# Performance work log

Hardware: AMD Instinct MI355X
Metric: run time of the kernel (lower is better)

The kernel has to match this reference:

```python
import jax, jax.numpy as jnp
import numpy as np

TOKEN_DIM = 768
HIDDEN_DIM = 384
PATCH_SCALE = 2
SELECTED_RATIO = 0.15


def setup_inputs() -> dict:
    key = jax.random.key(0)
    ks = jax.random.split(key, 12)
    B, T, D = 32, 1024, TOKEN_DIM
    Thr = T * PATCH_SCALE * PATCH_SCALE  # 4096
    flat_dim = D * PATCH_SCALE * PATCH_SCALE  # 3072
    H = HIDDEN_DIM
    s = lambda fan_in: 1.0 / np.sqrt(fan_in)
    inp = {
        "base_tokens": jax.random.normal(ks[0], (B, T, D), jnp.float32),
        "highres_tokens": jax.random.normal(ks[1], (B, Thr, D), jnp.float32),
        "selection_scores": jax.random.normal(ks[2], (B, T), jnp.float32),
        # local_refine: Linear(flat_dim,H) -> GELU -> Linear(H,D)
        "W1": jax.random.uniform(ks[3], (flat_dim, H), jnp.float32, -s(flat_dim), s(flat_dim)),
        "b1": jax.random.uniform(ks[4], (H,), jnp.float32, -s(flat_dim), s(flat_dim)),
        "W2": jax.random.uniform(ks[5], (H, D), jnp.float32, -s(H), s(H)),
        "b2": jax.random.uniform(ks[6], (D,), jnp.float32, -s(H), s(H)),
        # blend_gate: Linear(2D+1,H) -> SiLU -> Linear(H,1)
        "Wg1": jax.random.uniform(ks[7], (2 * D + 1, H), jnp.float32, -s(2 * D + 1), s(2 * D + 1)),
        "bg1": jax.random.uniform(ks[8], (H,), jnp.float32, -s(2 * D + 1), s(2 * D + 1)),
        "Wg2": jax.random.uniform(ks[9], (H, 1), jnp.float32, -s(H), s(H)),
        "bg2": jax.random.uniform(ks[10], (1,), jnp.float32, -s(H), s(H)),
    }
    return inp


def reference(base_tokens, highres_tokens, selection_scores,
              W1, b1, W2, b2, Wg1, bg1, Wg2, bg2):
    B, T, D = base_tokens.shape
    S = PATCH_SCALE
    g = int(round(np.sqrt(T)))  # coarse grid side
    # strided patch reshape: [B, g, S, g, S, D] -> [B, g, g, S, S, D] -> [B, T, S*S*D]
    local = highres_tokens.reshape(B, g, S, g, S, D)
    local = local.transpose(0, 1, 3, 2, 4, 5).reshape(B, T, S * S * D)
    # local refine MLP (exact-erf GELU matches torch nn.GELU default)
    h = jax.nn.gelu(jnp.einsum('btf,fh->bth', local, W1) + b1, approximate=False)
    refined_local = jnp.einsum('bth,hd->btd', h, W2) + b2
    # blend gate
    gate_in = jnp.concatenate([base_tokens, refined_local, selection_scores[..., None]], axis=-1)
    hg = jax.nn.silu(jnp.einsum('btf,fh->bth', gate_in, Wg1) + bg1)
    gate = jax.nn.sigmoid(jnp.einsum('bth,ho->bto', hg, Wg2) + bg2)  # [B, T, 1]
    # top-k selection mask (static k)
    topk = max(1, int(round(T * SELECTED_RATIO)))
    topk_idx = jax.lax.top_k(selection_scores, topk)[1]  # [B, k]
    mask = jnp.zeros((B, T), base_tokens.dtype).at[jnp.arange(B)[:, None], topk_idx].set(1.0)
    refined = base_tokens + mask[..., None] * gate * (refined_local - base_tokens)
    return refined
```

## Files before the change

### kernel.cpp

```cpp
#include <hip/hip_runtime.h>
#include <cstdint>

#define NB    32
#define NTOK  1024
#define D_    768
#define NHR   4096
#define HID   384
#define KSEL  154
#define MSEL  4928
#define MT_   77
#define FLAT  3072

typedef short  s16x8 __attribute__((ext_vector_type(8)));
typedef unsigned short u16x8 __attribute__((ext_vector_type(8)));
typedef unsigned short u16x4 __attribute__((ext_vector_type(4)));
typedef float  f32x4 __attribute__((ext_vector_type(4)));

__device__ inline unsigned short f2bf(float f) {
    uint32_t u = __builtin_bit_cast(uint32_t, f);
    u += 0x7FFFu + ((u >> 16) & 1u);
    return (unsigned short)(u >> 16);
}
__device__ inline float bf2f(unsigned short h) {
    uint32_t u = ((uint32_t)h) << 16;
    return __builtin_bit_cast(float, u);
}
__device__ inline s16x8 cvt8(const float* __restrict__ p) {
    float4 v0 = *(const float4*)p, v1 = *(const float4*)(p + 4);
    s16x8 r;
    r[0]=(short)f2bf(v0.x); r[1]=(short)f2bf(v0.y); r[2]=(short)f2bf(v0.z); r[3]=(short)f2bf(v0.w);
    r[4]=(short)f2bf(v1.x); r[5]=(short)f2bf(v1.y); r[6]=(short)f2bf(v1.z); r[7]=(short)f2bf(v1.w);
    return r;
}

#define OFF_SEL   0
#define OFF_RMAP  32768
#define OFF_GPART 163840
#define OFF_W1T   401408
#define OFF_W2T   2760704
#define OFF_WG1T  3350528
#define OFF_ABASE 4530176
#define OFF_H     12099584
#define OFF_RL    15884288
#define DOUT_P0   32505856
#define PSTRIDE   (MSEL * HID)

__global__ __launch_bounds__(1024) void prep_kernel(
    const float* __restrict__ scores, int* __restrict__ sel, int* __restrict__ rmap,
    const float* __restrict__ W1, const float* __restrict__ W2, const float* __restrict__ Wg1,
    unsigned short* __restrict__ W1t, unsigned short* __restrict__ W2t,
    unsigned short* __restrict__ Wg1t)
{
    __shared__ float s[NTOK];
    __shared__ int cnt;
    __shared__ unsigned short T[4][64][66];
    const int bid = blockIdx.x;
    if (bid < NB) {
        const int b = bid;
        const int t = threadIdx.x;
        s[t] = scores[b * NTOK + t];
        if (t == 0) cnt = 0;
        __syncthreads();
        float v = s[t];
        int rank = 0;
        for (int j = 0; j < NTOK; ++j) {
            float vj = s[j];
            rank += (vj > v) || (vj == v && j < t);
        }
        int rm = -1;
        if (rank < KSEL) {
            int pos = atomicAdd(&cnt, 1);
            rm = b * KSEL + pos;
            sel[rm] = t;
        }
        rmap[b * NTOK + t] = rm;
    } else {
        const int g = threadIdx.x >> 8;
        const int tid = threadIdx.x & 255;
        const int tile = (bid - NB) * 4 + g;
        const float* src; unsigned short* dst; int K, N, kt, nt;
        if (tile < 288)      { src = W1;  dst = W1t;  K = FLAT; N = HID; nt = tile % 6;  kt = tile / 6;  }
        else if (tile < 360) { int l = tile - 288; src = W2;  dst = W2t;  K = HID;  N = D_;  nt = l % 12; kt = l / 12; }
        else                 { int l = tile - 360; src = Wg1; dst = Wg1t; K = 1536; N = HID; nt = l % 6;  kt = l / 6;  }
        const int k0 = kt * 64, n0 = nt * 64;
        {
            const int ln = tid & 63, kc = tid >> 6;
            #pragma unroll
            for (int j = 0; j < 16; ++j)
                T[g][ln][kc * 16 + j] = f2bf(src[(uint64_t)(k0 + kc * 16 + j) * N + n0 + ln]);
        }
        __syncthreads();
        {
            const int row = tid >> 2, c0 = (tid & 3) * 16;
            u16x8 v0, v1;
            #pragma unroll
            for (int p = 0; p < 8; ++p) { v0[p] = T[g][row][c0 + p]; v1[p] = T[g][row][c0 + 8 + p]; }
            *(u16x8*)(dst + (uint64_t)(n0 + row) * K + k0 + c0) = v0;
            *(u16x8*)(dst + (uint64_t)(n0 + row) * K + k0 + c0 + 8) = v1;
        }
    }
}

__global__ __launch_bounds__(256) void gather_kernel(
    const int* __restrict__ sel, const float* __restrict__ highres,
    const float* __restrict__ base,
    unsigned short* __restrict__ Aloc, unsigned short* __restrict__ Abase) {
    const int r = blockIdx.x;
    const int b = r / KSEL;
    const int t = sel[r];
    const int gy = t >> 5, gx = t & 31;
    for (int ch = threadIdx.x; ch < 480; ch += 256) {
        if (ch < 384) {
            int k8 = ch * 8;
            int p = k8 / D_;
            int col = k8 - p * D_;
            int hr = (gy * 2 + (p >> 1)) * 64 + gx * 2 + (p & 1);
            s16x8 v = cvt8(highres + ((uint64_t)b * NHR + hr) * D_ + col);
            *(s16x8*)(Aloc + (uint64_t)r * FLAT + k8) = v;
        } else {
            int col = (ch - 384) * 8;
            s16x8 v = cvt8(base + ((uint64_t)b * NTOK + t) * D_ + col);
            *(s16x8*)(Abase + (uint64_t)r * D_ + col) = v;
        }
    }
}

template <int MODE>
__global__ __launch_bounds__(256) void gemm_mfma(
    const unsigned short* __restrict__ A0,
    const unsigned short* __restrict__ A1,
    const unsigned short* __restrict__ Bt,
    const float* __restrict__ bias,
    const int* __restrict__ sel,
    const float* __restrict__ scores,
    const float* __restrict__ WgLast,
    const float* __restrict__ Wg2,
    void* __restrict__ Cout,
    float* __restrict__ Pout,
    float* __restrict__ gpart)
{
    constexpr int K = MODE == 0 ? FLAT : (MODE == 1 ? HID : 2 * D_);
    constexpr int N = MODE == 1 ? D_ : HID;
    constexpr int BN = (MODE == 2) ? 64 : 128;
    constexpr int NFRAG = BN / 32;
    constexpr int NT = N / BN;
    constexpr int KLEN = (MODE == 0) ? 1024 : K;
    constexpr int NSTEP = KLEN / 64;
    constexpr int NSPLIT = (MODE == 0) ? 3 : 1;

    const int lin = blockIdx.x;
    const int xcd = lin & 7;
    int j = lin >> 3;
    const int ntile = j % NT; j /= NT;
    const int mhi = j % 10;
    const int split = j / 10;
    const int mt = mhi * 8 + xcd;
    if (mt >= MT_) return;
    const int m0 = mt * 64;
    const int n0 = ntile * BN;
    const int kb = split * KLEN;

    __shared__ unsigned short As[2][64 * 64];
    __shared__ unsigned short Bs[2][BN * 64];
    __shared__ float scv[64];

    const int tid = threadIdx.x;
    const int lane = tid & 63;
    const int wid = tid >> 6;
    const int wm = wid >> 1;
    const int wn = wid & 1;

    if (MODE == 2 && tid < 64) {
        int r = m0 + tid, b = r / KSEL, t = sel[r];
        scv[tid] = scores[b * NTOK + t];
    }

    const int sr0 = tid >> 3;
    const int sc0 = tid & 7;

    s16x8 aR[2], bR[NFRAG];
    auto loadTile = [&](int k0) {
        #pragma unroll
        for (int half = 0; half < 2; ++half) {
            int r = sr0 + half * 32;
            int k = k0 + sc0 * 8;
            const unsigned short* p;
            if (MODE == 0)      p = A0 + (uint64_t)(m0 + r) * FLAT + k;
            else if (MODE == 1) p = A0 + (uint64_t)(m0 + r) * HID + k;
            else {
                p = (k < D_) ? (A0 + (uint64_t)(m0 + r) * D_ + k)
                             : (A1 + (uint64_t)(m0 + r) * D_ + (k - D_));
            }
            aR[half] = *(const s16x8*)p;
        }
        #pragma unroll
        for (int it = 0; it < NFRAG; ++it) {
            int r = it * 32 + sr0;
            bR[it] = *(const s16x8*)(Bt + (uint64_t)(n0 + r) * K + k0 + sc0 * 8);
        }
    };
    auto writeTile = [&](int buf) {
        #pragma unroll
        for (int half = 0; half < 2; ++half) {
            int r = sr0 + half * 32;
            int c = sc0 ^ (r & 7);
            *(s16x8*)&As[buf][r * 64 + c * 8] = aR[half];
        }
        #pragma unroll
        for (int it = 0; it < NFRAG; ++it) {
            int r = it * 32 + sr0;
            int c = sc0 ^ (r & 7);
            *(s16x8*)&Bs[buf][r * 64 + c * 8] = bR[it];
        }
    };

    f32x4 acc[2][NFRAG];
    #pragma unroll
    for (int i = 0; i < 2; ++i)
        #pragma unroll
        for (int jj = 0; jj < NFRAG; ++jj) acc[i][jj] = (f32x4){0.f, 0.f, 0.f, 0.f};

    loadTile(kb);
    writeTile(0);
    __syncthreads();
    if (NSTEP > 1) loadTile(kb + 64);

    int cur = 0;
    for (int t = 0; t < NSTEP; ++t) {
        #pragma unroll
        for (int kk = 0; kk < 2; ++kk) {
            s16x8 af[2], bfr[NFRAG];
            #pragma unroll
            for (int i = 0; i < 2; ++i) {
                int row = wm * 32 + i * 16 + (lane & 15);
                int cch = (kk * 4 + (lane >> 4)) ^ (row & 7);
                af[i] = *(const s16x8*)&As[cur][row * 64 + cch * 8];
            }
            #pragma unroll
            for (int jj = 0; jj < NFRAG; ++jj) {
                int nrow = wn * (BN / 2) + jj * 16 + (lane & 15);
                int cch = (kk * 4 + (lane >> 4)) ^ (nrow & 7);
                bfr[jj] = *(const s16x8*)&Bs[cur][nrow * 64 + cch * 8];
            }
            #pragma unroll
            for (int i = 0; i < 2; ++i)
                #pragma unroll
                for (int jj = 0; jj < NFRAG; ++jj)
                    acc[i][jj] = __builtin_amdgcn_mfma_f32_16x16x32_bf16(af[i], bfr[jj], acc[i][jj], 0, 0, 0);
        }
        if (t + 1 < NSTEP) {
            writeTile(cur ^ 1);
            __syncthreads();
            if (t + 2 < NSTEP) loadTile(kb + (t + 2) * 64);
            cur ^= 1;
        }
    }

    if (MODE == 2) {
        float wg2v[2] = { Wg2[n0 + wn * 32 + (lane & 15)],
                          Wg2[n0 + wn * 32 + 16 + (lane & 15)] };
        float psum[2][4];
        #pragma unroll
        for (int i = 0; i < 2; ++i)
            #pragma unroll
            for (int reg = 0; reg < 4; ++reg) psum[i][reg] = 0.f;
        #pragma unroll
        for (int i = 0; i < 2; ++i) {
            #pragma unroll
            for (int jj = 0; jj < 2; ++jj) {
                #pragma unroll
                for (int reg = 0; reg < 4; ++reg) {
                    int m = m0 + wm * 32 + i * 16 + (lane >> 4) * 4 + reg;
                    int n = n0 + wn * 32 + jj * 16 + (lane & 15);
                    float x = acc[i][jj][reg] + bias[n] + scv[m - m0] * WgLast[n];
                    x = x / (1.0f + __expf(-x));
                    psum[i][reg] += x * wg2v[jj];
                }
            }
        }
        #pragma unroll
        for (int mask = 1; mask < 16; mask <<= 1)
            #pragma unroll
            for (int i = 0; i < 2; ++i)
                #pragma unroll
                for (int reg = 0; reg < 4; ++reg)
                    psum[i][reg] += __shfl_xor(psum[i][reg], mask);
        if ((lane & 15) == 0) {
            #pragma unroll
            for (int i = 0; i < 2; ++i)
                #pragma unroll
                for (int reg = 0; reg < 4; ++reg) {
                    int m = m0 + wm * 32 + i * 16 + (lane >> 4) * 4 + reg;
                    gpart[m * 12 + ntile * 2 + wn] = psum[i][reg];
                }
        }
        return;
    }
    float* P = (MODE == 0) ? (Pout + (uint64_t)split * PSTRIDE) : nullptr;
    #pragma unroll
    for (int i = 0; i < 2; ++i)
        #pragma unroll
        for (int jj = 0; jj < NFRAG; ++jj)
            #pragma unroll
            for (int reg = 0; reg < 4; ++reg) {
                int m = m0 + wm * 32 + i * 16 + (lane >> 4) * 4 + reg;
                int n = n0 + wn * (BN / 2) + jj * 16 + (lane & 15);
                if (MODE == 0) {
                    P[(uint64_t)m * HID + n] = acc[i][jj][reg];
                } else {
                    float x = acc[i][jj][reg] + bias[n];
                    ((unsigned short*)Cout)[(uint64_t)m * D_ + n] = f2bf(x);
                }
            }
}

__global__ __launch_bounds__(256) void combine_kernel(
    const float* __restrict__ P, const float* __restrict__ b1,
    unsigned short* __restrict__ h)
{
    const int idx = (blockIdx.x * 256 + threadIdx.x) * 8;
    const int col = idx % HID;
    float4 a0 = *(const float4*)(P + idx),               a1 = *(const float4*)(P + idx + 4);
    float4 c0 = *(const float4*)(P + PSTRIDE + idx),     c1 = *(const float4*)(P + PSTRIDE + idx + 4);
    float4 d0 = *(const float4*)(P + 2 * PSTRIDE + idx), d1 = *(const float4*)(P + 2 * PSTRIDE + idx + 4);
    float4 bb0 = *(const float4*)(b1 + col), bb1 = *(const float4*)(b1 + col + 4);
    float xs[8] = { a0.x + c0.x + d0.x + bb0.x, a0.y + c0.y + d0.y + bb0.y,
                    a0.z + c0.z + d0.z + bb0.z, a0.w + c0.w + d0.w + bb0.w,
                    a1.x + c1.x + d1.x + bb1.x, a1.y + c1.y + d1.y + bb1.y,
                    a1.z + c1.z + d1.z + bb1.z, a1.w + c1.w + d1.w + bb1.w };
    u16x8 v;
    #pragma unroll
    for (int p = 0; p < 8; ++p) {
        float x = xs[p];
        x = 0.5f * x * (1.0f + erff(x * 0.70710678118654752f));
        v[p] = f2bf(x);
    }
    *(u16x8*)(h + idx) = v;
}

__global__ __launch_bounds__(256) void finalize_kernel(
    const int* __restrict__ rmap,
    const float* __restrict__ gpart, const float* __restrict__ bg2,
    const float* __restrict__ base, const unsigned short* __restrict__ rl,
    float* __restrict__ out)
{
    const int lane = threadIdx.x & 63;
    const int row = blockIdx.x * 4 + (threadIdx.x >> 6);
    const int rm = rmap[row];

    const uint64_t bo = (uint64_t)row * D_;
    const float4* b4 = (const float4*)(base + bo);
    float4* o4 = (float4*)(out + bo);

    if (rm < 0) {
        #pragma unroll
        for (int i = 0; i < 3; ++i) o4[lane + 64 * i] = b4[lane + 64 * i];
        return;
    }
    const float4* gp = (const float4*)(gpart + (uint64_t)rm * 12);
    float4 g0 = gp[0], g1 = gp[1], g2 = gp[2];
    float sum = g0.x + g0.y + g0.z + g0.w + g1.x + g1.y + g1.z + g1.w
              + g2.x + g2.y + g2.z + g2.w + bg2[0];
    float gate = 1.0f / (1.0f + __expf(-sum));

    const u16x4* r4 = (const u16x4*)(rl + (uint64_t)rm * D_);
    #pragma unroll
    for (int i = 0; i < 3; ++i) {
        int idx = lane + 64 * i;
        float4 bb = b4[idx];
        u16x4 rr = r4[idx];
        float4 oo;
        oo.x = bb.x + gate * (bf2f(rr[0]) - bb.x);
        oo.y = bb.y + gate * (bf2f(rr[1]) - bb.y);
        oo.z = bb.z + gate * (bf2f(rr[2]) - bb.z);
        oo.w = bb.w + gate * (bf2f(rr[3]) - bb.w);
        o4[idx] = oo;
    }
}

extern "C" void kernel_launch(void* const* d_in, const int* in_sizes, int n_in,
                              void* d_out, int out_size, void* d_ws, size_t ws_size,
                              hipStream_t stream) {
    const float* base   = (const float*)d_in[0];
    const float* hires  = (const float*)d_in[1];
    const float* scores = (const float*)d_in[2];
    const float* W1  = (const float*)d_in[3];
    const float* b1  = (const float*)d_in[4];
    const float* W2  = (const float*)d_in[5];
    const float* b2  = (const float*)d_in[6];
    const float* Wg1 = (const float*)d_in[7];
    const float* bg1 = (const float*)d_in[8];
    const float* Wg2 = (const float*)d_in[9];
    const float* bg2 = (const float*)d_in[10];
    float* out = (float*)d_out;

    char* ws = (char*)d_ws;
    int*            sel   = (int*)(ws + OFF_SEL);
    int*            rmap  = (int*)(ws + OFF_RMAP);
    float*          gpart = (float*)(ws + OFF_GPART);
    unsigned short* W1t   = (unsigned short*)(ws + OFF_W1T);
    unsigned short* W2t   = (unsigned short*)(ws + OFF_W2T);
    unsigned short* Wg1t  = (unsigned short*)(ws + OFF_WG1T);
    unsigned short* Abase = (unsigned short*)(ws + OFF_ABASE);
    unsigned short* h     = (unsigned short*)(ws + OFF_H);
    unsigned short* rl    = (unsigned short*)(ws + OFF_RL);
    unsigned short* Aloc  = (unsigned short*)d_out;
    float*          P0    = (float*)((char*)d_out + DOUT_P0);

    prep_kernel<<<dim3(NB + 126), dim3(1024), 0, stream>>>(scores, sel, rmap,
                                                           W1, W2, Wg1, W1t, W2t, Wg1t);
    gather_kernel<<<dim3(MSEL), dim3(256), 0, stream>>>(sel, hires, base, Aloc, Abase);
    gemm_mfma<0><<<dim3(8 * 10 * 3 * 3), dim3(256), 0, stream>>>(
        Aloc, nullptr, W1t, nullptr, nullptr, nullptr, nullptr, nullptr, nullptr, P0, nullptr);
    combine_kernel<<<dim3(924), dim3(256), 0, stream>>>(P0, b1, h);
    gemm_mfma<1><<<dim3(8 * 10 * 6), dim3(256), 0, stream>>>(
        h, nullptr, W2t, b2, nullptr, nullptr, nullptr, nullptr, rl, nullptr, nullptr);
    gemm_mfma<2><<<dim3(8 * 10 * 6), dim3(256), 0, stream>>>(
        Abase, rl, Wg1t, bg1, sel, scores, Wg1 + (uint64_t)1536 * HID, Wg2,
        nullptr, nullptr, gpart);
    finalize_kernel<<<dim3(NB * NTOK / 4), dim3(256), 0, stream>>>(rmap, gpart, bg2, base, rl, out);
}
```

Baseline: 148.4 us.

## Fuse selected-token gather and bf16 conversion into GEMM A-tile loads

Result: slower. 152.3 us (+2.6%).

```diff
diff --git a/kernel.cpp b/kernel.cpp
--- a/kernel.cpp
+++ b/kernel.cpp
@@ -39,10 +39,8 @@
 #define OFF_W1T   401408
 #define OFF_W2T   2760704
 #define OFF_WG1T  3350528
-#define OFF_ABASE 4530176
-#define OFF_H     12099584
-#define OFF_RL    15884288
-#define DOUT_P0   32505856
+#define OFF_H     4530176
+#define OFF_RL    8314880
 #define PSTRIDE   (MSEL * HID)
 
 __global__ __launch_bounds__(1024) void prep_kernel(
@@ -101,34 +99,10 @@
     }
 }
 
-__global__ __launch_bounds__(256) void gather_kernel(
-    const int* __restrict__ sel, const float* __restrict__ highres,
-    const float* __restrict__ base,
-    unsigned short* __restrict__ Aloc, unsigned short* __restrict__ Abase) {
-    const int r = blockIdx.x;
-    const int b = r / KSEL;
-    const int t = sel[r];
-    const int gy = t >> 5, gx = t & 31;
-    for (int ch = threadIdx.x; ch < 480; ch += 256) {
-        if (ch < 384) {
-            int k8 = ch * 8;
-            int p = k8 / D_;
-            int col = k8 - p * D_;
-            int hr = (gy * 2 + (p >> 1)) * 64 + gx * 2 + (p & 1);
-            s16x8 v = cvt8(highres + ((uint64_t)b * NHR + hr) * D_ + col);
-            *(s16x8*)(Aloc + (uint64_t)r * FLAT + k8) = v;
-        } else {
-            int col = (ch - 384) * 8;
-            s16x8 v = cvt8(base + ((uint64_t)b * NTOK + t) * D_ + col);
-            *(s16x8*)(Abase + (uint64_t)r * D_ + col) = v;
-        }
-    }
-}
-
 template <int MODE>
 __global__ __launch_bounds__(256) void gemm_mfma(
-    const unsigned short* __restrict__ A0,
-    const unsigned short* __restrict__ A1,
+    const float* __restrict__ Araw,
+    const unsigned short* __restrict__ Abf,
     const unsigned short* __restrict__ Bt,
     const float* __restrict__ bias,
     const int* __restrict__ sel,
@@ -146,7 +120,6 @@
     constexpr int NT = N / BN;
     constexpr int KLEN = (MODE == 0) ? 1024 : K;
     constexpr int NSTEP = KLEN / 64;
-    constexpr int NSPLIT = (MODE == 0) ? 3 : 1;
 
     const int lin = blockIdx.x;
     const int xcd = lin & 7;
@@ -162,6 +135,7 @@
 
     __shared__ unsigned short As[2][64 * 64];
     __shared__ unsigned short Bs[2][BN * 64];
+    __shared__ uint32_t offT[64 * 4];
     __shared__ float scv[64];
 
     const int tid = threadIdx.x;
@@ -170,10 +144,23 @@
     const int wm = wid >> 1;
     const int wn = wid & 1;
 
-    if (MODE == 2 && tid < 64) {
-        int r = m0 + tid, b = r / KSEL, t = sel[r];
-        scv[tid] = scores[b * NTOK + t];
-    }
+    if (tid < 64) {
+        int r = m0 + tid;
+        if (MODE == 0) {
+            int b = r / KSEL, t = sel[r];
+            int gy = t >> 5, gx = t & 31;
+            #pragma unroll
+            for (int p = 0; p < 4; ++p) {
+                int hr = (gy * 2 + (p >> 1)) * 64 + gx * 2 + (p & 1);
+                offT[tid * 4 + p] = (uint32_t)(b * NHR + hr) * D_;
+            }
+        } else if (MODE == 2) {
+            int b = r / KSEL, t = sel[r];
+            offT[tid * 4] = (uint32_t)(b * NTOK + t) * D_;
+            scv[tid] = scores[b * NTOK + t];
+        }
+    }
+    if (MODE != 1) __syncthreads();
 
     const int sr0 = tid >> 3;
     const int sc0 = tid & 7;
@@ -184,14 +171,15 @@
         for (int half = 0; half < 2; ++half) {
             int r = sr0 + half * 32;
             int k = k0 + sc0 * 8;
-            const unsigned short* p;
-            if (MODE == 0)      p = A0 + (uint64_t)(m0 + r) * FLAT + k;
-            else if (MODE == 1) p = A0 + (uint64_t)(m0 + r) * HID + k;
-            else {
-                p = (k < D_) ? (A0 + (uint64_t)(m0 + r) * D_ + k)
-                             : (A1 + (uint64_t)(m0 + r) * D_ + (k - D_));
-            }
-            aR[half] = *(const s16x8*)p;
+            if (MODE == 0) {
+                int p = k0 / D_;
+                aR[half] = cvt8(Araw + offT[r * 4 + p] + (k - p * D_));
+            } else if (MODE == 1) {
+                aR[half] = *(const s16x8*)(Abf + (uint64_t)(m0 + r) * HID + k);
+            } else {
+                if (k < D_) aR[half] = cvt8(Araw + offT[r * 4] + k);
+                else        aR[half] = *(const s16x8*)(Abf + (uint64_t)(m0 + r) * D_ + (k - D_));
+            }
         }
         #pragma unroll
         for (int it = 0; it < NFRAG; ++it) {
@@ -401,22 +389,19 @@
     unsigned short* W1t   = (unsigned short*)(ws + OFF_W1T);
     unsigned short* W2t   = (unsigned short*)(ws + OFF_W2T);
     unsigned short* Wg1t  = (unsigned short*)(ws + OFF_WG1T);
-    unsigned short* Abase = (unsigned short*)(ws + OFF_ABASE);
     unsigned short* h     = (unsigned short*)(ws + OFF_H);
     unsigned short* rl    = (unsigned short*)(ws + OFF_RL);
-    unsigned short* Aloc  = (unsigned short*)d_out;
-    float*          P0    = (float*)((char*)d_out + DOUT_P0);
+    float*          P0    = (float*)d_out;
 
     prep_kernel<<<dim3(NB + 126), dim3(1024), 0, stream>>>(scores, sel, rmap,
                                                            W1, W2, Wg1, W1t, W2t, Wg1t);
-    gather_kernel<<<dim3(MSEL), dim3(256), 0, stream>>>(sel, hires, base, Aloc, Abase);
     gemm_mfma<0><<<dim3(8 * 10 * 3 * 3), dim3(256), 0, stream>>>(
-        Aloc, nullptr, W1t, nullptr, nullptr, nullptr, nullptr, nullptr, nullptr, P0, nullptr);
+        hires, nullptr, W1t, nullptr, sel, nullptr, nullptr, nullptr, nullptr, P0, nullptr);
     combine_kernel<<<dim3(924), dim3(256), 0, stream>>>(P0, b1, h);
     gemm_mfma<1><<<dim3(8 * 10 * 6), dim3(256), 0, stream>>>(
-        h, nullptr, W2t, b2, nullptr, nullptr, nullptr, nullptr, rl, nullptr, nullptr);
+        nullptr, h, W2t, b2, nullptr, nullptr, nullptr, nullptr, rl, nullptr, nullptr);
     gemm_mfma<2><<<dim3(8 * 10 * 6), dim3(256), 0, stream>>>(
-        Abase, rl, Wg1t, bg1, sel, scores, Wg1 + (uint64_t)1536 * HID, Wg2,
+        base, rl, Wg1t, bg1, sel, scores, Wg1 + (uint64_t)1536 * HID, Wg2,
         nullptr, nullptr, gpart);
     finalize_kernel<<<dim3(NB * NTOK / 4), dim3(256), 0, stream>>>(rmap, gpart, bg2, base, rl, out);
 }
```

## Overlap base-to-output copy with GEMM kernels via extra copy blocks

Applied to the files above, without the earlier changes.

After: 157.6 us. 1.06x slower.

```diff
diff --git a/kernel.cpp b/kernel.cpp
--- a/kernel.cpp
+++ b/kernel.cpp
@@ -42,7 +42,7 @@
 #define OFF_ABASE 4530176
 #define OFF_H     12099584
 #define OFF_RL    15884288
-#define DOUT_P0   32505856
+#define PBASE     77955072
 #define PSTRIDE   (MSEL * HID)
 
 __global__ __launch_bounds__(1024) void prep_kernel(
@@ -137,7 +137,9 @@
     const float* __restrict__ Wg2,
     void* __restrict__ Cout,
     float* __restrict__ Pout,
-    float* __restrict__ gpart)
+    float* __restrict__ gpart,
+    const float* __restrict__ CpySrc,
+    float* __restrict__ CpyDst)
 {
     constexpr int K = MODE == 0 ? FLAT : (MODE == 1 ? HID : 2 * D_);
     constexpr int N = MODE == 1 ? D_ : HID;
@@ -146,9 +148,22 @@
     constexpr int NT = N / BN;
     constexpr int KLEN = (MODE == 0) ? 1024 : K;
     constexpr int NSTEP = KLEN / 64;
-    constexpr int NSPLIT = (MODE == 0) ? 3 : 1;
+    constexpr int GB  = (MODE == 0) ? 720 : 480;
+    constexpr int CB  = (MODE == 0) ? 768 : 512;
+    constexpr int CLO = (MODE == 0) ? 9856 : (MODE == 1 ? 0 : 25376);
+    constexpr int CNR = (MODE == 0) ? 15520 : (MODE == 1 ? 9856 : 7392);
 
     const int lin = blockIdx.x;
+    if (lin >= GB) {
+        const int cb = lin - GB;
+        const float4* src = (const float4*)CpySrc + (uint64_t)CLO * 192;
+        float4* dst = (float4*)CpyDst + (uint64_t)CLO * 192;
+        const int n4 = CNR * 192;
+        for (int idx = cb * 256 + threadIdx.x; idx < n4; idx += CB * 256)
+            dst[idx] = src[idx];
+        return;
+    }
+
     const int xcd = lin & 7;
     int j = lin >> 3;
     const int ntile = j % NT; j /= NT;
@@ -338,32 +353,27 @@
     *(u16x8*)(h + idx) = v;
 }
 
-__global__ __launch_bounds__(256) void finalize_kernel(
-    const int* __restrict__ rmap,
+__global__ __launch_bounds__(256) void blend_kernel(
+    const int* __restrict__ sel,
     const float* __restrict__ gpart, const float* __restrict__ bg2,
     const float* __restrict__ base, const unsigned short* __restrict__ rl,
     float* __restrict__ out)
 {
     const int lane = threadIdx.x & 63;
-    const int row = blockIdx.x * 4 + (threadIdx.x >> 6);
-    const int rm = rmap[row];
-
-    const uint64_t bo = (uint64_t)row * D_;
-    const float4* b4 = (const float4*)(base + bo);
-    float4* o4 = (float4*)(out + bo);
-
-    if (rm < 0) {
-        #pragma unroll
-        for (int i = 0; i < 3; ++i) o4[lane + 64 * i] = b4[lane + 64 * i];
-        return;
-    }
-    const float4* gp = (const float4*)(gpart + (uint64_t)rm * 12);
+    const int r = blockIdx.x * 4 + (threadIdx.x >> 6);
+    const int b = r / KSEL;
+    const int t = sel[r];
+
+    const float4* gp = (const float4*)(gpart + (uint64_t)r * 12);
     float4 g0 = gp[0], g1 = gp[1], g2 = gp[2];
     float sum = g0.x + g0.y + g0.z + g0.w + g1.x + g1.y + g1.z + g1.w
               + g2.x + g2.y + g2.z + g2.w + bg2[0];
     float gate = 1.0f / (1.0f + __expf(-sum));
 
-    const u16x4* r4 = (const u16x4*)(rl + (uint64_t)rm * D_);
+    const uint64_t bo = ((uint64_t)b * NTOK + t) * D_;
+    const float4* b4 = (const float4*)(base + bo);
+    const u16x4* r4 = (const u16x4*)(rl + (uint64_t)r * D_);
+    float4* o4 = (float4*)(out + bo);
     #pragma unroll
     for (int i = 0; i < 3; ++i) {
         int idx = lane + 64 * i;
@@ -405,18 +415,20 @@
     unsigned short* h     = (unsigned short*)(ws + OFF_H);
     unsigned short* rl    = (unsigned short*)(ws + OFF_RL);
     unsigned short* Aloc  = (unsigned short*)d_out;
-    float*          P0    = (float*)((char*)d_out + DOUT_P0);
+    float*          P0    = (float*)((char*)d_out + PBASE);
 
     prep_kernel<<<dim3(NB + 126), dim3(1024), 0, stream>>>(scores, sel, rmap,
                                                            W1, W2, Wg1, W1t, W2t, Wg1t);
     gather_kernel<<<dim3(MSEL), dim3(256), 0, stream>>>(sel, hires, base, Aloc, Abase);
-    gemm_mfma<0><<<dim3(8 * 10 * 3 * 3), dim3(256), 0, stream>>>(
-        Aloc, nullptr, W1t, nullptr, nullptr, nullptr, nullptr, nullptr, nullptr, P0, nullptr);
+    gemm_mfma<0><<<dim3(720 + 768), dim3(256), 0, stream>>>(
+        Aloc, nullptr, W1t, nullptr, nullptr, nullptr, nullptr, nullptr, nullptr, P0, nullptr,
+        base, out);
     combine_kernel<<<dim3(924), dim3(256), 0, stream>>>(P0, b1, h);
-    gemm_mfma<1><<<dim3(8 * 10 * 6), dim3(256), 0, stream>>>(
-        h, nullptr, W2t, b2, nullptr, nullptr, nullptr, nullptr, rl, nullptr, nullptr);
-    gemm_mfma<2><<<dim3(8 * 10 * 6), dim3(256), 0, stream>>>(
+    gemm_mfma<1><<<dim3(480 + 512), dim3(256), 0, stream>>>(
+        h, nullptr, W2t, b2, nullptr, nullptr, nullptr, nullptr, rl, nullptr, nullptr,
+        base, out);
+    gemm_mfma<2><<<dim3(480 + 512), dim3(256), 0, stream>>>(
         Abase, rl, Wg1t, bg1, sel, scores, Wg1 + (uint64_t)1536 * HID, Wg2,
-        nullptr, nullptr, gpart);
-    finalize_kernel<<<dim3(NB * NTOK / 4), dim3(256), 0, stream>>>(rmap, gpart, bg2, base, rl, out);
-}
+        nullptr, nullptr, gpart, base, out);
+    blend_kernel<<<dim3(MSEL / 4), dim3(256), 0, stream>>>(sel, gpart, bg2, base, rl, out);
+}
```

## Fold W2 into gate weights so gate GEMM runs concurrently with refine GEMM

Applied to the files above, without the earlier changes.

Measured after the change: 166.3 us. +12.1%, slower.

```diff
diff --git a/kernel.cpp b/kernel.cpp
--- a/kernel.cpp
+++ b/kernel.cpp
@@ -42,6 +42,8 @@
 #define OFF_ABASE 4530176
 #define OFF_H     12099584
 #define OFF_RL    15884288
+#define OFF_WF    23453696
+#define OFF_BC    23748608
 #define DOUT_P0   32505856
 #define PSTRIDE   (MSEL * HID)
 
@@ -101,35 +103,14 @@
     }
 }
 
-__global__ __launch_bounds__(256) void gather_kernel(
-    const int* __restrict__ sel, const float* __restrict__ highres,
-    const float* __restrict__ base,
-    unsigned short* __restrict__ Aloc, unsigned short* __restrict__ Abase) {
-    const int r = blockIdx.x;
-    const int b = r / KSEL;
-    const int t = sel[r];
-    const int gy = t >> 5, gx = t & 31;
-    for (int ch = threadIdx.x; ch < 480; ch += 256) {
-        if (ch < 384) {
-            int k8 = ch * 8;
-            int p = k8 / D_;
-            int col = k8 - p * D_;
-            int hr = (gy * 2 + (p >> 1)) * 64 + gx * 2 + (p & 1);
-            s16x8 v = cvt8(highres + ((uint64_t)b * NHR + hr) * D_ + col);
-            *(s16x8*)(Aloc + (uint64_t)r * FLAT + k8) = v;
-        } else {
-            int col = (ch - 384) * 8;
-            s16x8 v = cvt8(base + ((uint64_t)b * NTOK + t) * D_ + col);
-            *(s16x8*)(Abase + (uint64_t)r * D_ + col) = v;
-        }
-    }
-}
-
 template <int MODE>
-__global__ __launch_bounds__(256) void gemm_mfma(
+__device__ __forceinline__ void gemm_body(
+    int lin,
     const unsigned short* __restrict__ A0,
     const unsigned short* __restrict__ A1,
-    const unsigned short* __restrict__ Bt,
+    const unsigned short* __restrict__ B0,
+    const unsigned short* __restrict__ B1,
+    const float* __restrict__ Braw,
     const float* __restrict__ bias,
     const int* __restrict__ sel,
     const float* __restrict__ scores,
@@ -137,32 +118,33 @@
     const float* __restrict__ Wg2,
     void* __restrict__ Cout,
     float* __restrict__ Pout,
-    float* __restrict__ gpart)
-{
-    constexpr int K = MODE == 0 ? FLAT : (MODE == 1 ? HID : 2 * D_);
-    constexpr int N = MODE == 1 ? D_ : HID;
-    constexpr int BN = (MODE == 2) ? 64 : 128;
+    float* __restrict__ gpart,
+    unsigned short* __restrict__ AsS,
+    unsigned short* __restrict__ BsS,
+    float* __restrict__ scv)
+{
+    constexpr int BN    = (MODE == 0 || MODE == 1) ? 128 : 64;
     constexpr int NFRAG = BN / 32;
-    constexpr int NT = N / BN;
-    constexpr int KLEN = (MODE == 0) ? 1024 : K;
+    constexpr int N     = (MODE == 1) ? D_ : HID;
+    constexpr int NT    = N / BN;
+    constexpr int KLEN  = (MODE == 0) ? 1024 : (MODE == 1) ? HID : (MODE == 2) ? 1152 : D_;
     constexpr int NSTEP = KLEN / 64;
-    constexpr int NSPLIT = (MODE == 0) ? 3 : 1;
-
-    const int lin = blockIdx.x;
-    const int xcd = lin & 7;
-    int j = lin >> 3;
-    const int ntile = j % NT; j /= NT;
-    const int mhi = j % 10;
-    const int split = j / 10;
-    const int mt = mhi * 8 + xcd;
-    if (mt >= MT_) return;
+
+    int mt, ntile, split;
+    if constexpr (MODE == 3) {
+        mt = lin / 6; ntile = lin % 6; split = 0;
+    } else {
+        const int xcd = lin & 7;
+        int j = lin >> 3;
+        ntile = j % NT; j /= NT;
+        const int mhi = j % 10;
+        split = j / 10;
+        mt = mhi * 8 + xcd;
+        if (mt >= MT_) return;
+    }
     const int m0 = mt * 64;
     const int n0 = ntile * BN;
     const int kb = split * KLEN;
-
-    __shared__ unsigned short As[2][64 * 64];
-    __shared__ unsigned short Bs[2][BN * 64];
-    __shared__ float scv[64];
 
     const int tid = threadIdx.x;
     const int lane = tid & 63;
@@ -184,33 +166,47 @@
         for (int half = 0; half < 2; ++half) {
             int r = sr0 + half * 32;
             int k = k0 + sc0 * 8;
-            const unsigned short* p;
-            if (MODE == 0)      p = A0 + (uint64_t)(m0 + r) * FLAT + k;
-            else if (MODE == 1) p = A0 + (uint64_t)(m0 + r) * HID + k;
-            else {
-                p = (k < D_) ? (A0 + (uint64_t)(m0 + r) * D_ + k)
-                             : (A1 + (uint64_t)(m0 + r) * D_ + (k - D_));
-            }
-            aR[half] = *(const s16x8*)p;
+            if constexpr (MODE == 0) {
+                aR[half] = *(const s16x8*)(A0 + (uint64_t)(m0 + r) * FLAT + k);
+            } else if constexpr (MODE == 1) {
+                aR[half] = *(const s16x8*)(A0 + (uint64_t)(m0 + r) * HID + k);
+            } else if constexpr (MODE == 2) {
+                if (k < D_) aR[half] = *(const s16x8*)(A0 + (uint64_t)(m0 + r) * D_ + k);
+                else        aR[half] = *(const s16x8*)(A1 + (uint64_t)(m0 + r) * HID + (k - D_));
+            } else {
+                aR[half] = *(const s16x8*)(A0 + (uint64_t)(m0 + r) * 1536 + k);
+            }
         }
         #pragma unroll
         for (int it = 0; it < NFRAG; ++it) {
             int r = it * 32 + sr0;
-            bR[it] = *(const s16x8*)(Bt + (uint64_t)(n0 + r) * K + k0 + sc0 * 8);
+            int k = k0 + sc0 * 8;
+            if constexpr (MODE == 0) {
+                bR[it] = *(const s16x8*)(B0 + (uint64_t)(n0 + r) * FLAT + k);
+            } else if constexpr (MODE == 1) {
+                bR[it] = *(const s16x8*)(B0 + (uint64_t)(n0 + r) * HID + k);
+            } else if constexpr (MODE == 2) {
+                if (k < D_) bR[it] = *(const s16x8*)(B0 + (uint64_t)(n0 + r) * 1536 + k);
+                else        bR[it] = *(const s16x8*)(B1 + (uint64_t)(n0 + r) * HID + (k - D_));
+            } else {
+                bR[it] = cvt8(Braw + (uint64_t)(n0 + r) * D_ + k);
+            }
         }
     };
     auto writeTile = [&](int buf) {
+        unsigned short* As = AsS + buf * 4096;
+        unsigned short* Bs = BsS + buf * (BN * 64);
         #pragma unroll
         for (int half = 0; half < 2; ++half) {
             int r = sr0 + half * 32;
             int c = sc0 ^ (r & 7);
-            *(s16x8*)&As[buf][r * 64 + c * 8] = aR[half];
+            *(s16x8*)&As[r * 64 + c * 8] = aR[half];
         }
         #pragma unroll
         for (int it = 0; it < NFRAG; ++it) {
             int r = it * 32 + sr0;
             int c = sc0 ^ (r & 7);
-            *(s16x8*)&Bs[buf][r * 64 + c * 8] = bR[it];
+            *(s16x8*)&Bs[r * 64 + c * 8] = bR[it];
         }
     };
 
@@ -227,6 +223,8 @@
 
     int cur = 0;
     for (int t = 0; t < NSTEP; ++t) {
+        const unsigned short* As = AsS + cur * 4096;
+        const unsigned short* Bs = BsS + cur * (BN * 64);
         #pragma unroll
         for (int kk = 0; kk < 2; ++kk) {
             s16x8 af[2], bfr[NFRAG];
@@ -234,13 +232,13 @@
             for (int i = 0; i < 2; ++i) {
                 int row = wm * 32 + i * 16 + (lane & 15);
                 int cch = (kk * 4 + (lane >> 4)) ^ (row & 7);
-                af[i] = *(const s16x8*)&As[cur][row * 64 + cch * 8];
+                af[i] = *(const s16x8*)&As[row * 64 + cch * 8];
             }
             #pragma unroll
             for (int jj = 0; jj < NFRAG; ++jj) {
                 int nrow = wn * (BN / 2) + jj * 16 + (lane & 15);
                 int cch = (kk * 4 + (lane >> 4)) ^ (nrow & 7);
-                bfr[jj] = *(const s16x8*)&Bs[cur][nrow * 64 + cch * 8];
+                bfr[jj] = *(const s16x8*)&Bs[nrow * 64 + cch * 8];
             }
             #pragma unroll
             for (int i = 0; i < 2; ++i)
@@ -256,7 +254,7 @@
         }
     }
 
-    if (MODE == 2) {
+    if constexpr (MODE == 2) {
         float wg2v[2] = { Wg2[n0 + wn * 32 + (lane & 15)],
                           Wg2[n0 + wn * 32 + 16 + (lane & 15)] };
         float psum[2][4];
@@ -296,7 +294,6 @@
         }
         return;
     }
-    float* P = (MODE == 0) ? (Pout + (uint64_t)split * PSTRIDE) : nullptr;
     #pragma unroll
     for (int i = 0; i < 2; ++i)
         #pragma unroll
@@ -305,13 +302,71 @@
             for (int reg = 0; reg < 4; ++reg) {
                 int m = m0 + wm * 32 + i * 16 + (lane >> 4) * 4 + reg;
                 int n = n0 + wn * (BN / 2) + jj * 16 + (lane & 15);
-                if (MODE == 0) {
-                    P[(uint64_t)m * HID + n] = acc[i][jj][reg];
-                } else {
+                if constexpr (MODE == 0) {
+                    Pout[(uint64_t)split * PSTRIDE + (uint64_t)m * HID + n] = acc[i][jj][reg];
+                } else if constexpr (MODE == 1) {
                     float x = acc[i][jj][reg] + bias[n];
                     ((unsigned short*)Cout)[(uint64_t)m * D_ + n] = f2bf(x);
+                } else {
+                    ((unsigned short*)Cout)[(uint64_t)m * HID + n] = f2bf(acc[i][jj][reg]);
                 }
             }
+}
+
+__global__ __launch_bounds__(256) void gworker_kernel(
+    const int* __restrict__ sel, const float* __restrict__ highres,
+    const float* __restrict__ base,
+    unsigned short* __restrict__ Aloc, unsigned short* __restrict__ Abase,
+    const unsigned short* __restrict__ Wg1t, const float* __restrict__ W2,
+    const float* __restrict__ bg1, const float* __restrict__ b2,
+    unsigned short* __restrict__ WF, float* __restrict__ bias_comb)
+{
+    __shared__ unsigned short AsS[2 * 4096];
+    __shared__ unsigned short BsS[2 * 4096];
+    const int bid = blockIdx.x;
+    if (bid < MSEL) {
+        const int r = bid;
+        const int b = r / KSEL;
+        const int t = sel[r];
+        const int gy = t >> 5, gx = t & 31;
+        for (int ch = threadIdx.x; ch < 480; ch += 256) {
+            if (ch < 384) {
+                int k8 = ch * 8;
+                int p = k8 / D_;
+                int col = k8 - p * D_;
+                int hr = (gy * 2 + (p >> 1)) * 64 + gx * 2 + (p & 1);
+                s16x8 v = cvt8(highres + ((uint64_t)b * NHR + hr) * D_ + col);
+                *(s16x8*)(Aloc + (uint64_t)r * FLAT + k8) = v;
+            } else {
+                int col = (ch - 384) * 8;
+                s16x8 v = cvt8(base + ((uint64_t)b * NTOK + t) * D_ + col);
+                *(s16x8*)(Abase + (uint64_t)r * D_ + col) = v;
+            }
+        }
+        return;
+    }
+    const int wb = bid - MSEL;
+    gemm_body<3>(wb, Wg1t + 768, nullptr, nullptr, nullptr, W2, nullptr,
+                 nullptr, nullptr, nullptr, nullptr, WF, nullptr, nullptr,
+                 AsS, BsS, nullptr);
+    if (wb % 6 == 0 && threadIdx.x < 64) {
+        int n = (wb / 6) * 64 + threadIdx.x;
+        float s = bg1[n];
+        const unsigned short* wr = Wg1t + (uint64_t)n * 1536 + 768;
+        for (int d = 0; d < 768; ++d) s += b2[d] * bf2f(wr[d]);
+        bias_comb[n] = s;
+    }
+}
+
+__global__ __launch_bounds__(256) void gemm0_kernel(
+    const unsigned short* __restrict__ Aloc, const unsigned short* __restrict__ W1t,
+    float* __restrict__ Pout)
+{
+    __shared__ unsigned short AsS[2 * 4096];
+    __shared__ unsigned short BsS[2 * 8192];
+    gemm_body<0>(blockIdx.x, Aloc, nullptr, W1t, nullptr, nullptr, nullptr,
+                 nullptr, nullptr, nullptr, nullptr, nullptr, Pout, nullptr,
+                 AsS, BsS, nullptr);
 }
 
 __global__ __launch_bounds__(256) void combine_kernel(
@@ -338,6 +393,29 @@
     *(u16x8*)(h + idx) = v;
 }
 
+__global__ __launch_bounds__(256) void gemm12_kernel(
+    const unsigned short* __restrict__ h, const unsigned short* __restrict__ W2t,
+    const float* __restrict__ b2,
+    const unsigned short* __restrict__ Abase, const unsigned short* __restrict__ Wg1t,
+    const unsigned short* __restrict__ WF, const float* __restrict__ bias_comb,
+    const int* __restrict__ sel, const float* __restrict__ scores,
+    const float* __restrict__ WgLast, const float* __restrict__ Wg2,
+    unsigned short* __restrict__ rl, float* __restrict__ gpart)
+{
+    __shared__ unsigned short AsS[2 * 4096];
+    __shared__ unsigned short BsS[2 * 8192];
+    __shared__ float scv[64];
+    if (blockIdx.x < 480) {
+        gemm_body<1>(blockIdx.x, h, nullptr, W2t, nullptr, nullptr, b2,
+                     nullptr, nullptr, nullptr, nullptr, rl, nullptr, nullptr,
+                     AsS, BsS, nullptr);
+    } else {
+        gemm_body<2>(blockIdx.x - 480, Abase, h, Wg1t, WF, nullptr, bias_comb,
+                     sel, scores, WgLast, Wg2, nullptr, nullptr, gpart,
+                     AsS, BsS, scv);
+    }
+}
+
 __global__ __launch_bounds__(256) void finalize_kernel(
     const int* __restrict__ rmap,
     const float* __restrict__ gpart, const float* __restrict__ bg2,
@@ -404,19 +482,19 @@
     unsigned short* Abase = (unsigned short*)(ws + OFF_ABASE);
     unsigned short* h     = (unsigned short*)(ws + OFF_H);
     unsigned short* rl    = (unsigned short*)(ws + OFF_RL);
+    unsigned short* WF    = (unsigned short*)(ws + OFF_WF);
+    float*          bcomb = (float*)(ws + OFF_BC);
     unsigned short* Aloc  = (unsigned short*)d_out;
     float*          P0    = (float*)((char*)d_out + DOUT_P0);
 
     prep_kernel<<<dim3(NB + 126), dim3(1024), 0, stream>>>(scores, sel, rmap,
                                                            W1, W2, Wg1, W1t, W2t, Wg1t);
-    gather_kernel<<<dim3(MSEL), dim3(256), 0, stream>>>(sel, hires, base, Aloc, Abase);
-    gemm_mfma<0><<<dim3(8 * 10 * 3 * 3), dim3(256), 0, stream>>>(
-        Aloc, nullptr, W1t, nullptr, nullptr, nullptr, nullptr, nullptr, nullptr, P0, nullptr);
+    gworker_kernel<<<dim3(MSEL + 36), dim3(256), 0, stream>>>(
+        sel, hires, base, Aloc, Abase, Wg1t, W2, bg1, b2, WF, bcomb);
+    gemm0_kernel<<<dim3(8 * 10 * 3 * 3), dim3(256), 0, stream>>>(Aloc, W1t, P0);
     combine_kernel<<<dim3(924), dim3(256), 0, stream>>>(P0, b1, h);
-    gemm_mfma<1><<<dim3(8 * 10 * 6), dim3(256), 0, stream>>>(
-        h, nullptr, W2t, b2, nullptr, nullptr, nullptr, nullptr, rl, nullptr, nullptr);
-    gemm_mfma<2><<<dim3(8 * 10 * 6), dim3(256), 0, stream>>>(
-        Abase, rl, Wg1t, bg1, sel, scores, Wg1 + (uint64_t)1536 * HID, Wg2,
-        nullptr, nullptr, gpart);
+    gemm12_kernel<<<dim3(480 + 480), dim3(256), 0, stream>>>(
+        h, W2t, b2, Abase, Wg1t, WF, bcomb, sel, scores,
+        Wg1 + (uint64_t)1536 * HID, Wg2, rl, gpart);
     finalize_kernel<<<dim3(NB * NTOK / 4), dim3(256), 0, stream>>>(rmap, gpart, bg2, base, rl, out);
 }
```
